# Kernel optimization log

Hardware: AMD Instinct MI355X
Metric: run time of the kernel (lower is better)

The kernel has to match this reference:

```python
import jax, jax.numpy as jnp
import numpy as np

KEYS = 11     # inference_keys: number of heatmap channels / keypoints
NSTACK = 4
B, H, W = 16, 128, 128


def setup_inputs() -> dict:
    key = jax.random.key(0)
    k1, k2, k3 = jax.random.split(key, 3)
    combined_preds = jax.random.normal(k1, (B, NSTACK, 2 * KEYS, H, W), dtype=jnp.float32)
    heatmaps = jax.random.uniform(k2, (B, KEYS, H, W), dtype=jnp.float32)
    # labels[..., 9] and [..., 10] are keypoint coords; scale to [0, 160) so some
    # fall outside [0, H)=[0,128) and exercise the validity-mask branch.
    labels = jax.random.uniform(k3, (B, KEYS, 11), dtype=jnp.float32) * 160.0
    return {"combined_preds": combined_preds, "heatmaps": heatmaps, "labels": labels}


def reference(combined_preds, heatmaps, labels):
    keys = KEYS
    hm = combined_preds[:, :, :keys]          # [B, S, K, H, W] heatmap preds
    lb = combined_preds[:, :, keys:]          # [B, S, K, H, W] label preds
    b, s, k, m, n = hm.shape                  # m = H, n = W (code uses m for both // and %)

    # HeatmapLoss per stack, vectorized over the stack dim
    heat_loss = ((hm - heatmaps[:, None]) ** 2).sum(axis=(2, 3, 4))  # [B, S]

    # LabelLoss, fully vectorized over (B, S, K)
    flat = hm.reshape(b, s, k, m * n)
    index = jnp.argmax(flat, axis=-1)         # [B, S, K]
    x = index // m                            # matches int(index / m) in original
    y = index % m
    # a[x, y] where a is the [H, W] heatmap -> flat[x * W + y]
    a_xy = jnp.take_along_axis(flat, (x * n + y)[..., None], axis=-1)[..., 0]

    pred = lb.reshape(b, s, k, -1)            # [B, S, K, H*W]
    lab = labels[:, None]                     # [B, 1, K, 11] broadcast over stacks

    gx, gy = lab[..., 9], lab[..., 10]
    valid = (gx > 0) & (gy > 0) & (gx < m) & (gy < n)

    xf = x.astype(pred.dtype)
    yf = y.astype(pred.dtype)
    xy_loss = (gx + lab[..., 7] - xf - pred[..., 7]) ** 2 \
            + (gy + lab[..., 8] - yf - pred[..., 8]) ** 2
    conf_loss = (1.0 - a_xy) ** 2
    class_loss = ((pred[..., 0:7] - lab[..., 0:7]) ** 2).sum(axis=-1)

    per_kp = jnp.where(valid, class_loss + xy_loss + conf_loss, 0.0)  # [B, S, K]
    label_loss = per_kp.sum(axis=-1)                                   # [B, S]

    return heat_loss, label_loss
```

## Files before the change

### kernel.cpp

```cpp
#include <hip/hip_runtime.h>
#include <math.h>

#define KEYS 11
#define NSTACK 4
#define NB 16
#define HH 128
#define WW 128
#define HW (HH * WW)
#define CHUNKS 4
#define CHUNK_F4 1024
#define NSLICE (NB * NSTACK * KEYS)
#define NPART (NSLICE * CHUNKS)


__global__ __launch_bounds__(256) void kp_partial_kernel(
    const float* __restrict__ cp,
    const float* __restrict__ heat,
    float* __restrict__ ws)
{
    const int bid   = blockIdx.x;
    const int c     = bid & 3;
    const int slice = bid >> 2;
    const int k  = slice % KEYS;
    const int bs = slice / KEYS;
    const int b  = bs >> 2;

    const float4* __restrict__ hm4 = (const float4*)(cp + ((size_t)(bs * (2 * KEYS) + k)) * HW);
    const float4* __restrict__ ht4 = (const float4*)(heat + ((size_t)(b * KEYS + k)) * HW);

    const int tid = threadIdx.x;
    float sum  = 0.0f;
    float vmax = -INFINITY;
    int   imax = 0;

    #pragma unroll
    for (int j = 0; j < 4; j++) {
        int i = c * CHUNK_F4 + tid + j * 256;
        float4 a = hm4[i];
        float4 h = ht4[i];
        float d0 = a.x - h.x, d1 = a.y - h.y, d2 = a.z - h.z, d3 = a.w - h.w;
        sum += d0 * d0 + d1 * d1 + d2 * d2 + d3 * d3;
        int base = i * 4;
        if (a.x > vmax) { vmax = a.x; imax = base;     }
        if (a.y > vmax) { vmax = a.y; imax = base + 1; }
        if (a.z > vmax) { vmax = a.z; imax = base + 2; }
        if (a.w > vmax) { vmax = a.w; imax = base + 3; }
    }

    #pragma unroll
    for (int off = 32; off > 0; off >>= 1) {
        float ov = __shfl_down(vmax, off);
        int   oi = __shfl_down(imax, off);
        float os = __shfl_down(sum,  off);
        sum += os;
        if (ov > vmax || (ov == vmax && oi < imax)) { vmax = ov; imax = oi; }
    }

    __shared__ float s_sum[4];
    __shared__ float s_v[4];
    __shared__ int   s_i[4];
    const int wave = tid >> 6;
    if ((tid & 63) == 0) { s_sum[wave] = sum; s_v[wave] = vmax; s_i[wave] = imax; }
    __syncthreads();

    if (tid == 0) {
        #pragma unroll
        for (int w = 1; w < 4; w++) {
            sum += s_sum[w];
            if (s_v[w] > vmax || (s_v[w] == vmax && s_i[w] < imax)) {
                vmax = s_v[w]; imax = s_i[w];
            }
        }
        ws[bid]        = sum;
        ws[4096 + bid] = vmax;
        ((int*)ws)[8192 + bid] = imax;
    }
}

__global__ __launch_bounds__(768) void kp_final_kernel(
    const float* __restrict__ cp,
    const float* __restrict__ lab,
    const float* __restrict__ ws,
    float* __restrict__ out)
{
    __shared__ float sh[NSLICE];
    __shared__ float sl[NSLICE];

    const int t = threadIdx.x;
    if (t < NSLICE) {
        const int slice = t;
        const int k  = slice % KEYS;
        const int bs = slice / KEYS;
        const int b  = bs >> 2;

        float sum  = 0.0f;
        float vmax = -INFINITY;
        int   imax = 0;
        #pragma unroll
        for (int c = 0; c < CHUNKS; c++) {
            int p = slice * CHUNKS + c;
            float v = ws[4096 + p];
            if (v > vmax) { vmax = v; imax = ((const int*)ws)[8192 + p]; }
            sum += ws[p];
        }
        sh[t] = sum;

        const float* __restrict__ L  = lab + (size_t)(b * KEYS + k) * 11;
        float gx = L[9], gy = L[10];
        float loss = 0.0f;
        if ((gx > 0.0f) && (gy > 0.0f) && (gx < (float)HH) && (gy < (float)WW)) {
            const float* __restrict__ lb =
                cp + ((size_t)(bs * (2 * KEYS) + KEYS + k)) * HW;
            float xf = (float)(imax / WW);
            float yf = (float)(imax % WW);
            float dx = gx + L[7] - xf - lb[7];
            float dy = gy + L[8] - yf - lb[8];
            loss = dx * dx + dy * dy;
            float cm = 1.0f - vmax;
            loss += cm * cm;
            #pragma unroll
            for (int j = 0; j < 7; j++) {
                float d = lb[j] - L[j];
                loss += d * d;
            }
        }
        sl[t] = loss;
    }
    __syncthreads();

    if (t < 64) {
        float a = 0.0f, c = 0.0f;
        #pragma unroll
        for (int k = 0; k < KEYS; k++) {
            a += sh[t * KEYS + k];
            c += sl[t * KEYS + k];
        }
        out[t]      = a;
        out[64 + t] = c;
    }
}

extern "C" void kernel_launch(void* const* d_in, const int* in_sizes, int n_in,
                              void* d_out, int out_size, void* d_ws, size_t ws_size,
                              hipStream_t stream) {
    const float* cp   = (const float*)d_in[0];
    const float* heat = (const float*)d_in[1];
    const float* lab  = (const float*)d_in[2];
    float* out = (float*)d_out;
    float* ws  = (float*)d_ws;

    kp_partial_kernel<<<NPART, 256, 0, stream>>>(cp, heat, ws);
    kp_final_kernel<<<1, 768, 0, stream>>>(cp, lab, ws, out);
}
```

Before: 138.0 us.

## Fuse final reduction into partial kernel via last-block atomic counter

Merges the two-kernel reduction into one kernel. Each block publishes its partial sum and argmax with atomic stores, then increments a global counter, and the last block to finish performs the per-keypoint label loss and the final reduction. This removes the second kernel launch and its launch gap, but adds a memset before the kernel, a global atomic per block, and a serial tail executed by a single block of 256 threads.

```diff
diff --git a/kernel.cpp b/kernel.cpp
--- a/kernel.cpp
+++ b/kernel.cpp
@@ -13,10 +13,12 @@
 #define NPART (NSLICE * CHUNKS)
 
 
-__global__ __launch_bounds__(256) void kp_partial_kernel(
+__global__ __launch_bounds__(256) void kp_fused_kernel(
     const float* __restrict__ cp,
     const float* __restrict__ heat,
-    float* __restrict__ ws)
+    const float* __restrict__ lab,
+    float* __restrict__ ws,
+    float* __restrict__ out)
 {
     const int bid   = blockIdx.x;
     const int c     = bid & 3;
@@ -59,6 +61,7 @@
     __shared__ float s_sum[4];
     __shared__ float s_v[4];
     __shared__ int   s_i[4];
+    __shared__ int   s_last;
     const int wave = tid >> 6;
     if ((tid & 63) == 0) { s_sum[wave] = sum; s_v[wave] = vmax; s_i[wave] = imax; }
     __syncthreads();
@@ -71,52 +74,52 @@
                 vmax = s_v[w]; imax = s_i[w];
             }
         }
-        ws[bid]        = sum;
-        ws[4096 + bid] = vmax;
-        ((int*)ws)[8192 + bid] = imax;
+        __hip_atomic_store(&ws[1024 + bid],  sum,  __ATOMIC_RELAXED, __HIP_MEMORY_SCOPE_AGENT);
+        __hip_atomic_store(&ws[8192 + bid],  vmax, __ATOMIC_RELAXED, __HIP_MEMORY_SCOPE_AGENT);
+        __hip_atomic_store(&((int*)ws)[16384 + bid], imax, __ATOMIC_RELAXED, __HIP_MEMORY_SCOPE_AGENT);
+        __threadfence();
+        unsigned old = atomicAdd((unsigned*)ws, 1u);
+        s_last = (old == NPART - 1) ? 1 : 0;
     }
-}
+    __syncthreads();
+    if (s_last == 0) return;
 
-__global__ __launch_bounds__(768) void kp_final_kernel(
-    const float* __restrict__ cp,
-    const float* __restrict__ lab,
-    const float* __restrict__ ws,
-    float* __restrict__ out)
-{
+    __threadfence();
     __shared__ float sh[NSLICE];
     __shared__ float sl[NSLICE];
 
-    const int t = threadIdx.x;
-    if (t < NSLICE) {
-        const int slice = t;
-        const int k  = slice % KEYS;
-        const int bs = slice / KEYS;
-        const int b  = bs >> 2;
+    for (int t = tid; t < NSLICE; t += 256) {
+        const int kk  = t % KEYS;
+        const int bss = t / KEYS;
+        const int bb  = bss >> 2;
 
-        float sum  = 0.0f;
-        float vmax = -INFINITY;
-        int   imax = 0;
+        float fsum  = 0.0f;
+        float fvmax = -INFINITY;
+        int   fimax = 0;
         #pragma unroll
-        for (int c = 0; c < CHUNKS; c++) {
-            int p = slice * CHUNKS + c;
-            float v = ws[4096 + p];
-            if (v > vmax) { vmax = v; imax = ((const int*)ws)[8192 + p]; }
-            sum += ws[p];
+        for (int cc = 0; cc < CHUNKS; cc++) {
+            int p = t * CHUNKS + cc;
+            float v = __hip_atomic_load(&ws[8192 + p], __ATOMIC_RELAXED, __HIP_MEMORY_SCOPE_AGENT);
+            if (v > fvmax) {
+                fvmax = v;
+                fimax = __hip_atomic_load(&((int*)ws)[16384 + p], __ATOMIC_RELAXED, __HIP_MEMORY_SCOPE_AGENT);
+            }
+            fsum += __hip_atomic_load(&ws[1024 + p], __ATOMIC_RELAXED, __HIP_MEMORY_SCOPE_AGENT);
         }
-        sh[t] = sum;
+        sh[t] = fsum;
 
-        const float* __restrict__ L  = lab + (size_t)(b * KEYS + k) * 11;
+        const float* __restrict__ L = lab + (size_t)(bb * KEYS + kk) * 11;
         float gx = L[9], gy = L[10];
         float loss = 0.0f;
         if ((gx > 0.0f) && (gy > 0.0f) && (gx < (float)HH) && (gy < (float)WW)) {
             const float* __restrict__ lb =
-                cp + ((size_t)(bs * (2 * KEYS) + KEYS + k)) * HW;
-            float xf = (float)(imax / WW);
-            float yf = (float)(imax % WW);
+                cp + ((size_t)(bss * (2 * KEYS) + KEYS + kk)) * HW;
+            float xf = (float)(fimax / WW);
+            float yf = (float)(fimax % WW);
             float dx = gx + L[7] - xf - lb[7];
             float dy = gy + L[8] - yf - lb[8];
             loss = dx * dx + dy * dy;
-            float cm = 1.0f - vmax;
+            float cm = 1.0f - fvmax;
             loss += cm * cm;
             #pragma unroll
             for (int j = 0; j < 7; j++) {
@@ -128,15 +131,15 @@
     }
     __syncthreads();
 
-    if (t < 64) {
-        float a = 0.0f, c = 0.0f;
+    if (tid < 64) {
+        float a = 0.0f, cl = 0.0f;
         #pragma unroll
-        for (int k = 0; k < KEYS; k++) {
-            a += sh[t * KEYS + k];
-            c += sl[t * KEYS + k];
+        for (int kk = 0; kk < KEYS; kk++) {
+            a  += sh[tid * KEYS + kk];
+            cl += sl[tid * KEYS + kk];
         }
-        out[t]      = a;
-        out[64 + t] = c;
+        out[tid]      = a;
+        out[64 + tid] = cl;
     }
 }
 
@@ -149,6 +152,6 @@
     float* out = (float*)d_out;
     float* ws  = (float*)d_ws;
 
-    kp_partial_kernel<<<NPART, 256, 0, stream>>>(cp, heat, ws);
-    kp_final_kernel<<<1, 768, 0, stream>>>(cp, lab, ws, out);
+    hipMemsetAsync(ws, 0, 4, stream);
+    kp_fused_kernel<<<NPART, 256, 0, stream>>>(cp, heat, lab, ws, out);
 }
```

After: 258.1 us. +86.9%, slower.
